# Optimization experiments

Hardware: AMD Instinct MI355X
Metric: run time of the kernel (lower is better)

## Reference

```python
import jax, jax.numpy as jnp
import numpy as np

N, E, D, H = 20000, 320000, 300, 2
NEG_SLOPE = 0.2  # PyG GATConv default LeakyReLU slope


def setup_inputs() -> dict:
    key = jax.random.key(0)
    ks = jax.random.split(key, 8)
    return {
        "x": jax.random.normal(ks[0], (N, D), dtype=jnp.float32),
        "edge_index": jax.random.randint(ks[1], (2, E), 0, N, dtype=jnp.int64),
        "W": jax.random.normal(ks[2], (D, H, D), dtype=jnp.float32) * 0.05,
        "att_src": jax.random.normal(ks[3], (H, D), dtype=jnp.float32) * 0.05,
        "att_dst": jax.random.normal(ks[4], (H, D), dtype=jnp.float32) * 0.05,
        "bias": jax.random.normal(ks[5], (D,), dtype=jnp.float32) * 0.05,
        "lin_w": jax.random.normal(ks[6], (D, 1), dtype=jnp.float32) * 0.05,
        "lin_b": jax.random.normal(ks[7], (1,), dtype=jnp.float32) * 0.05,
    }


def reference(x, edge_index, W, att_src, att_dst, bias, lin_w, lin_b):
    n = x.shape[0]
    # add self-loops (PyG GATConv default)
    loops = jnp.arange(n, dtype=edge_index.dtype)
    src = jnp.concatenate([edge_index[0], loops])  # [E+N]
    dst = jnp.concatenate([edge_index[1], loops])
    # per-head linear projection: [N, H, D]
    xp = jnp.einsum('nd,dhe->nhe', x, W)
    # per-node attention logits [N, H]
    a_src = jnp.sum(xp * att_src, axis=-1)
    a_dst = jnp.sum(xp * att_dst, axis=-1)
    # per-edge score, LeakyReLU, segment softmax over incoming edges of dst
    e = jax.nn.leaky_relu(a_src[src] + a_dst[dst], NEG_SLOPE)  # [Et, H]
    emax = jax.ops.segment_max(e, dst, num_segments=n)  # self-loops ensure non-empty
    ee = jnp.exp(e - emax[dst])
    denom = jax.ops.segment_sum(ee, dst, num_segments=n)
    alpha = ee / denom[dst]  # [Et, H]
    # weighted scatter-add aggregation
    msg = xp[src] * alpha[:, :, None]  # [Et, H, D]
    out = jax.ops.segment_sum(msg, dst, num_segments=n)  # [N, H, D]
    out = out.mean(axis=1) + bias  # concat=False -> head average, then bias
    out = jax.nn.relu(out)
    return out @ lin_w + lin_b  # [N, 1]
```

## Files before the change

### kernel.cpp

```cpp
#include <hip/hip_runtime.h>
#include <math.h>

#define Nn 20000
#define Ee 320000
#define Dd 300
#define Hh 2
#define Cc 600
#define KP 320
#define MP 20096
#define NP 640
#define SQ 640

typedef _Float16 f16;
typedef __attribute__((ext_vector_type(8))) _Float16 f16x8;
typedef __attribute__((ext_vector_type(4))) _Float16 f16x4;
typedef __attribute__((ext_vector_type(4))) float f32x4;

__device__ __forceinline__ float lrelu(float x) { return x > 0.f ? x : 0.2f * x; }

#define GLDS16(src, dst)                                                            \
  __builtin_amdgcn_global_load_lds(                                                 \
      (const __attribute__((address_space(1))) unsigned int*)(src),                 \
      (__attribute__((address_space(3))) unsigned int*)(dst), 16, 0, 0)

__global__ __launch_bounds__(256) void k_pre2(const float* __restrict__ W,
                                              const float* __restrict__ att_src,
                                              const float* __restrict__ att_dst,
                                              f16* __restrict__ Wh, float* __restrict__ vatt,
                                              int* __restrict__ cnt, float* __restrict__ dsum) {
  int idx = blockIdx.x * 256 + threadIdx.x;
  if (idx < Nn) {
    cnt[idx] = 0;
    *(float2*)(dsum + 2 * idx) = make_float2(0.f, 0.f);
  }
  {
    int c = idx % NP, k0 = (idx / NP) * 4;
    f16x4 h;
#pragma unroll
    for (int j = 0; j < 4; ++j) {
      int k = k0 + j;
      h[j] = (f16)((k < Dd && c < Cc) ? W[(size_t)k * Cc + c] : 0.f);
    }
    *(f16x4*)(Wh + (size_t)c * KP + k0) = h;
  }
  int wid = idx >> 6, ln = idx & 63;
  if (wid < Dd) {
    float s0 = 0.f, s1 = 0.f, t0 = 0.f, t1 = 0.f;
    for (int e = ln; e < Dd; e += 64) {
      float w0 = W[(size_t)wid * Cc + e];
      float w1 = W[(size_t)wid * Cc + Dd + e];
      s0 += w0 * att_src[e];  s1 += w1 * att_src[Dd + e];
      t0 += w0 * att_dst[e];  t1 += w1 * att_dst[Dd + e];
    }
    for (int o = 32; o > 0; o >>= 1) {
      s0 += __shfl_down(s0, o, 64); s1 += __shfl_down(s1, o, 64);
      t0 += __shfl_down(t0, o, 64); t1 += __shfl_down(t1, o, 64);
    }
    if (ln == 0) {
      vatt[wid * 4 + 0] = s0; vatt[wid * 4 + 1] = s1;
      vatt[wid * 4 + 2] = t0; vatt[wid * 4 + 3] = t1;
    }
  }
}

__global__ __launch_bounds__(256) void k_pre1(const float* __restrict__ x,
                                              const float* __restrict__ vatt,
                                              const int* __restrict__ ei,
                                              f16* __restrict__ xh,
                                              float* __restrict__ a_src, float* __restrict__ a_dst,
                                              int* __restrict__ cnt) {
  int gid = blockIdx.x * 256 + threadIdx.x;
  if (gid < Ee) atomicAdd(&cnt[ei[Ee + gid]], 1);
  int wv = threadIdx.x >> 6, ln = threadIdx.x & 63;
  int n = blockIdx.x * 4 + wv;
  if (n >= MP) return;
  if (n >= Nn) {
#pragma unroll
    for (int k = 0; k < 5; ++k) xh[(size_t)n * KP + ln + 64 * k] = (f16)0.f;
    return;
  }
  const float* xr = x + (size_t)n * Dd;
  float s0 = 0.f, s1 = 0.f, t0 = 0.f, t1 = 0.f;
#pragma unroll
  for (int k = 0; k < 5; ++k) {
    int d = ln + 64 * k;
    float xv = 0.f;
    if (d < Dd) {
      xv = xr[d];
      float4 vv = *(const float4*)(vatt + d * 4);
      s0 += xv * vv.x; s1 += xv * vv.y; t0 += xv * vv.z; t1 += xv * vv.w;
    }
    xh[(size_t)n * KP + d] = (f16)xv;
  }
  for (int o = 32; o > 0; o >>= 1) {
    s0 += __shfl_down(s0, o, 64); s1 += __shfl_down(s1, o, 64);
    t0 += __shfl_down(t0, o, 64); t1 += __shfl_down(t1, o, 64);
  }
  if (ln == 0) {
    a_src[n * 2 + 0] = s0; a_src[n * 2 + 1] = s1;
    a_dst[n * 2 + 0] = t0; a_dst[n * 2 + 1] = t1;
  }
}

__global__ __launch_bounds__(256) void k_mm(const f16* __restrict__ xh, const f16* __restrict__ Wh,
                                            f16* __restrict__ xq) {
  __shared__ __align__(16) f16 As[128 * 32];
  __shared__ __align__(16) f16 Bs[128 * 32];
  int m0 = blockIdx.x * 128, n0 = blockIdx.y * 128;
  int tid = threadIdx.x, wv = tid >> 6, lane = tid & 63;
  int wr = wv >> 1, wc = wv & 1;

  int r0a = 32 * wv + (lane >> 2);
  int ca  = ((lane & 3) ^ ((r0a >> 1) & 3)) * 8;
  int r0b = r0a + 16;
  int cb  = ((lane & 3) ^ ((r0b >> 1) & 3)) * 8;

  f32x4 acc[4][4] = {};
  for (int ks = 0; ks < KP / 32; ++ks) {
    __syncthreads();
    GLDS16(xh + (size_t)(m0 + r0a) * KP + ks * 32 + ca, As + (32 * wv) * 32);
    GLDS16(xh + (size_t)(m0 + r0b) * KP + ks * 32 + cb, As + (32 * wv + 16) * 32);
    GLDS16(Wh + (size_t)(n0 + r0a) * KP + ks * 32 + ca, Bs + (32 * wv) * 32);
    GLDS16(Wh + (size_t)(n0 + r0b) * KP + ks * 32 + cb, Bs + (32 * wv + 16) * 32);
    __syncthreads();

    f16x8 af[4], bf[4];
#pragma unroll
    for (int i = 0; i < 4; ++i) {
      int rA = wr * 64 + i * 16 + (lane & 15);
      int sA = (lane >> 4) ^ ((rA >> 1) & 3);
      af[i] = *(const f16x8*)&As[rA * 32 + sA * 8];
      int rB = wc * 64 + i * 16 + (lane & 15);
      int sB = (lane >> 4) ^ ((rB >> 1) & 3);
      bf[i] = *(const f16x8*)&Bs[rB * 32 + sB * 8];
    }
#pragma unroll
    for (int i = 0; i < 4; ++i)
#pragma unroll
      for (int j = 0; j < 4; ++j)
        acc[i][j] = __builtin_amdgcn_mfma_f32_16x16x32_f16(af[i], bf[j], acc[i][j], 0, 0, 0);
  }

#pragma unroll
  for (int i = 0; i < 4; ++i) {
#pragma unroll
    for (int j = 0; j < 4; ++j) {
      int col = n0 + wc * 64 + j * 16 + (lane & 15);
      if (col < Cc) {
        int rbase = m0 + wr * 64 + i * 16 + ((lane >> 4) * 4);
#pragma unroll
        for (int r = 0; r < 4; ++r) {
          int row = rbase + r;
          if (row < Nn) xq[(size_t)row * SQ + col] = (f16)acc[i][j][r];
        }
      }
    }
  }
}

__global__ __launch_bounds__(1024) void k_scan(const int* __restrict__ cnt,
                                               int* __restrict__ offs, int* __restrict__ cur) {
  __shared__ int wsum[16];
  int t = threadIdx.x, wv = t >> 6, ln = t & 63;
  int i0 = t * 20;
  int v[20];
  int tot = 0;
  if (i0 < Nn) {
    const int4* p = (const int4*)(cnt + i0);
#pragma unroll
    for (int q = 0; q < 5; ++q) {
      int4 w = p[q];
      v[4 * q] = w.x; v[4 * q + 1] = w.y; v[4 * q + 2] = w.z; v[4 * q + 3] = w.w;
    }
#pragma unroll
    for (int j = 0; j < 20; ++j) tot += v[j];
  }
  int s = tot;
  for (int o = 1; o < 64; o <<= 1) {
    int u = __shfl_up(s, o, 64);
    if (ln >= o) s += u;
  }
  if (ln == 63) wsum[wv] = s;
  __syncthreads();
  if (wv == 0) {
    int w = (ln < 16) ? wsum[ln] : 0;
    for (int o = 1; o < 16; o <<= 1) {
      int u = __shfl_up(w, o, 64);
      if (ln >= o) w += u;
    }
    if (ln < 16) wsum[ln] = w;
  }
  __syncthreads();
  if (i0 < Nn) {
    int run = (wv > 0 ? wsum[wv - 1] : 0) + (s - tot);
#pragma unroll
    for (int j = 0; j < 20; ++j) {
      offs[i0 + j] = run;
      cur[i0 + j] = run;
      run += v[j];
    }
  }
  if (t == 0) offs[Nn] = wsum[15];
}

__global__ void k_scatter(const int* __restrict__ ei,
                          const float* __restrict__ a_src, const float* __restrict__ a_dst,
                          int* __restrict__ cur, float* __restrict__ dsum,
                          float4* __restrict__ erec) {
  int e = blockIdx.x * 256 + threadIdx.x;
  if (e < Ee) {
    int s = ei[e], d = ei[Ee + e];
    float2 av = *(const float2*)(a_src + 2 * s);
    float2 bv = *(const float2*)(a_dst + 2 * d);
    float e0 = __expf(lrelu(av.x + bv.x));
    float e1 = __expf(lrelu(av.y + bv.y));
    int pos = atomicAdd(&cur[d], 1);
    erec[pos] = make_float4(__int_as_float(s), e0, e1, 0.f);
    atomicAdd(&dsum[2 * d + 0], e0);
    atomicAdd(&dsum[2 * d + 1], e1);
  }
}

__global__ __launch_bounds__(256) void k_agg(const f16* __restrict__ xq,
    const float4* __restrict__ erec,
    const float* __restrict__ a_src, const float* __restrict__ a_dst,
    const float* __restrict__ dsum, const int* __restrict__ offs,
    const float* __restrict__ bias, const float* __restrict__ lin_w,
    const float* __restrict__ lin_b, float* __restrict__ out) {
  __shared__ float sAgg[4][600];
  int tid = threadIdx.x, wv = tid >> 6, ln = tid & 63;
  int n = blockIdx.x * 4 + wv;
  int beg = offs[n], deg = offs[n + 1] - beg;
  float2 adv = *(const float2*)(a_dst + 2 * n);
  float2 asv = *(const float2*)(a_src + 2 * n);
  float sw0 = __expf(lrelu(asv.x + adv.x));
  float sw1 = __expf(lrelu(asv.y + adv.y));
  float2 dv = *(const float2*)(dsum + 2 * n);
  float inv0 = 1.f / (dv.x + sw0), inv1 = 1.f / (dv.y + sw1);

  float acc[12] = {};
  auto addrow = [&](const f16* row, float p0, float p1) {
#pragma unroll
    for (int k = 0; k < 3; ++k) {
      int c = 4 * ln + 256 * k;
      if (c < Cc) {
        f16x4 hv = *(const f16x4*)(row + c);
        float p = (c < Dd) ? p0 : p1;
        acc[4 * k + 0] += p * (float)hv[0];
        acc[4 * k + 1] += p * (float)hv[1];
        acc[4 * k + 2] += p * (float)hv[2];
        acc[4 * k + 3] += p * (float)hv[3];
      }
    }
  };

  int j = 0;
  for (; j + 4 <= deg; j += 4) {
    float4 r0 = erec[beg + j + 0];
    float4 r1 = erec[beg + j + 1];
    float4 r2 = erec[beg + j + 2];
    float4 r3 = erec[beg + j + 3];
    addrow(xq + (size_t)__float_as_int(r0.x) * SQ, r0.y * inv0, r0.z * inv1);
    addrow(xq + (size_t)__float_as_int(r1.x) * SQ, r1.y * inv0, r1.z * inv1);
    addrow(xq + (size_t)__float_as_int(r2.x) * SQ, r2.y * inv0, r2.z * inv1);
    addrow(xq + (size_t)__float_as_int(r3.x) * SQ, r3.y * inv0, r3.z * inv1);
  }
  for (; j < deg; ++j) {
    float4 r = erec[beg + j];
    addrow(xq + (size_t)__float_as_int(r.x) * SQ, r.y * inv0, r.z * inv1);
  }
  addrow(xq + (size_t)n * SQ, sw0 * inv0, sw1 * inv1);

#pragma unroll
  for (int k = 0; k < 3; ++k) {
    int c = 4 * ln + 256 * k;
    if (c < Cc) {
#pragma unroll
      for (int q = 0; q < 4; ++q) sAgg[wv][c + q] = acc[4 * k + q];
    }
  }
  __syncthreads();

  float part = 0.f;
#pragma unroll
  for (int k = 0; k < 5; ++k) {
    int d = ln + 64 * k;
    if (d < Dd) {
      float v = 0.5f * (sAgg[wv][d] + sAgg[wv][d + Dd]) + bias[d];
      v = fmaxf(v, 0.f);
      part += v * lin_w[d];
    }
  }
  for (int o = 32; o > 0; o >>= 1) part += __shfl_xor(part, o, 64);
  if (ln == 0) out[n] = part + lin_b[0];
}

extern "C" void kernel_launch(void* const* d_in, const int* in_sizes, int n_in,
                              void* d_out, int out_size, void* d_ws, size_t ws_size,
                              hipStream_t stream) {
  const float* x       = (const float*)d_in[0];
  const int*   ei      = (const int*)d_in[1];
  const float* W       = (const float*)d_in[2];
  const float* att_src = (const float*)d_in[3];
  const float* att_dst = (const float*)d_in[4];
  const float* bias    = (const float*)d_in[5];
  const float* lin_w   = (const float*)d_in[6];
  const float* lin_b   = (const float*)d_in[7];
  float* out = (float*)d_out;

  char* ws = (char*)d_ws;
  size_t off = 0;
  auto alloc = [&](size_t bytes) {
    void* p = ws + off;
    off = (off + bytes + 255) & ~(size_t)255;
    return p;
  };
  f16*    xq    = (f16*)alloc((size_t)Nn * SQ * 2);
  f16*    xh    = (f16*)alloc((size_t)MP * KP * 2);
  f16*    Wh    = (f16*)alloc((size_t)NP * KP * 2);
  float*  vatt  = (float*)alloc((size_t)Dd * 4 * 4);
  float*  a_src = (float*)alloc((size_t)Nn * Hh * 4);
  float*  a_dst = (float*)alloc((size_t)Nn * Hh * 4);
  int*    cnt   = (int*)alloc((size_t)Nn * 4);
  int*    offs  = (int*)alloc((size_t)(Nn + 1) * 4);
  int*    cur   = (int*)alloc((size_t)Nn * 4);
  float*  dsum  = (float*)alloc((size_t)Nn * 2 * 4);
  float4* erec  = (float4*)alloc((size_t)Ee * 16);

  k_pre2<<<NP * (KP / 4) / 256, 256, 0, stream>>>(W, att_src, att_dst, Wh, vatt, cnt, dsum);
  k_pre1<<<MP / 4, 256, 0, stream>>>(x, vatt, ei, xh, a_src, a_dst, cnt);
  k_mm<<<dim3(MP / 128, NP / 128), 256, 0, stream>>>(xh, Wh, xq);
  k_scan<<<1, 1024, 0, stream>>>(cnt, offs, cur);
  k_scatter<<<(Ee + 255) / 256, 256, 0, stream>>>(ei, a_src, a_dst, cur, dsum, erec);
  k_agg<<<Nn / 4, 256, 0, stream>>>(xq, erec, a_src, a_dst, dsum, offs, bias, lin_w, lin_b, out);
}
```

Before: 246.8 us.

## Replace denominator atomics with per-node reduction and degree-sort aggregation nodes

Drops the per-edge atomic accumulation of softmax denominators; each wave in the aggregation kernel now sums its node's edge weights with a wave reduction. The scan kernel also builds a degree-bucketed permutation of nodes so aggregation blocks process nodes of similar degree. The aim is to cut atomic contention and reduce load imbalance between waves in a block. In exchange, aggregation reads the edge records an extra time and the single-block scan does more shared-memory atomic work.

Result: faster. 222.4 us (-9.9%).

```diff
diff --git a/kernel.cpp b/kernel.cpp
--- a/kernel.cpp
+++ b/kernel.cpp
@@ -27,12 +27,9 @@
                                               const float* __restrict__ att_src,
                                               const float* __restrict__ att_dst,
                                               f16* __restrict__ Wh, float* __restrict__ vatt,
-                                              int* __restrict__ cnt, float* __restrict__ dsum) {
+                                              int* __restrict__ cnt) {
   int idx = blockIdx.x * 256 + threadIdx.x;
-  if (idx < Nn) {
-    cnt[idx] = 0;
-    *(float2*)(dsum + 2 * idx) = make_float2(0.f, 0.f);
-  }
+  if (idx < Nn) cnt[idx] = 0;
   {
     int c = idx % NP, k0 = (idx / NP) * 4;
     f16x4 h;
@@ -159,8 +156,11 @@
 }
 
 __global__ __launch_bounds__(1024) void k_scan(const int* __restrict__ cnt,
-                                               int* __restrict__ offs, int* __restrict__ cur) {
+                                               int* __restrict__ offs, int* __restrict__ cur,
+                                               int* __restrict__ perm) {
   __shared__ int wsum[16];
+  __shared__ int dhist[64];
+  __shared__ int dcur[64];
   int t = threadIdx.x, wv = t >> 6, ln = t & 63;
   int i0 = t * 20;
   int v[20];
@@ -175,6 +175,7 @@
 #pragma unroll
     for (int j = 0; j < 20; ++j) tot += v[j];
   }
+  if (t < 64) dhist[t] = 0;
   int s = tot;
   for (int o = 1; o < 64; o <<= 1) {
     int u = __shfl_up(s, o, 64);
@@ -182,6 +183,10 @@
   }
   if (ln == 63) wsum[wv] = s;
   __syncthreads();
+  if (i0 < Nn) {
+#pragma unroll
+    for (int j = 0; j < 20; ++j) atomicAdd(&dhist[min(v[j], 63)], 1);
+  }
   if (wv == 0) {
     int w = (ln < 16) ? wsum[ln] : 0;
     for (int o = 1; o < 16; o <<= 1) {
@@ -191,6 +196,16 @@
     if (ln < 16) wsum[ln] = w;
   }
   __syncthreads();
+  if (wv == 0) {
+    int h = dhist[ln];
+    int sc = h;
+    for (int o = 1; o < 64; o <<= 1) {
+      int u = __shfl_up(sc, o, 64);
+      if (ln >= o) sc += u;
+    }
+    dcur[ln] = sc - h;
+  }
+  __syncthreads();
   if (i0 < Nn) {
     int run = (wv > 0 ? wsum[wv - 1] : 0) + (s - tot);
 #pragma unroll
@@ -198,6 +213,8 @@
       offs[i0 + j] = run;
       cur[i0 + j] = run;
       run += v[j];
+      int pos = atomicAdd(&dcur[min(v[j], 63)], 1);
+      perm[pos] = i0 + j;
     }
   }
   if (t == 0) offs[Nn] = wsum[15];
@@ -205,8 +222,7 @@
 
 __global__ void k_scatter(const int* __restrict__ ei,
                           const float* __restrict__ a_src, const float* __restrict__ a_dst,
-                          int* __restrict__ cur, float* __restrict__ dsum,
-                          float4* __restrict__ erec) {
+                          int* __restrict__ cur, float4* __restrict__ erec) {
   int e = blockIdx.x * 256 + threadIdx.x;
   if (e < Ee) {
     int s = ei[e], d = ei[Ee + e];
@@ -216,27 +232,34 @@
     float e1 = __expf(lrelu(av.y + bv.y));
     int pos = atomicAdd(&cur[d], 1);
     erec[pos] = make_float4(__int_as_float(s), e0, e1, 0.f);
-    atomicAdd(&dsum[2 * d + 0], e0);
-    atomicAdd(&dsum[2 * d + 1], e1);
   }
 }
 
 __global__ __launch_bounds__(256) void k_agg(const f16* __restrict__ xq,
-    const float4* __restrict__ erec,
+    const float4* __restrict__ erec, const int* __restrict__ perm,
     const float* __restrict__ a_src, const float* __restrict__ a_dst,
-    const float* __restrict__ dsum, const int* __restrict__ offs,
+    const int* __restrict__ offs,
     const float* __restrict__ bias, const float* __restrict__ lin_w,
     const float* __restrict__ lin_b, float* __restrict__ out) {
   __shared__ float sAgg[4][600];
   int tid = threadIdx.x, wv = tid >> 6, ln = tid & 63;
-  int n = blockIdx.x * 4 + wv;
+  int n = perm[blockIdx.x * 4 + wv];
   int beg = offs[n], deg = offs[n + 1] - beg;
   float2 adv = *(const float2*)(a_dst + 2 * n);
   float2 asv = *(const float2*)(a_src + 2 * n);
   float sw0 = __expf(lrelu(asv.x + adv.x));
   float sw1 = __expf(lrelu(asv.y + adv.y));
-  float2 dv = *(const float2*)(dsum + 2 * n);
-  float inv0 = 1.f / (dv.x + sw0), inv1 = 1.f / (dv.y + sw1);
+
+  float t0 = 0.f, t1 = 0.f;
+  for (int i = ln; i < deg; i += 64) {
+    float4 r = erec[beg + i];
+    t0 += r.y; t1 += r.z;
+  }
+  for (int o = 32; o > 0; o >>= 1) {
+    t0 += __shfl_xor(t0, o, 64);
+    t1 += __shfl_xor(t1, o, 64);
+  }
+  float inv0 = 1.f / (t0 + sw0), inv1 = 1.f / (t1 + sw1);
 
   float acc[12] = {};
   auto addrow = [&](const f16* row, float p0, float p1) {
@@ -324,13 +347,13 @@
   int*    cnt   = (int*)alloc((size_t)Nn * 4);
   int*    offs  = (int*)alloc((size_t)(Nn + 1) * 4);
   int*    cur   = (int*)alloc((size_t)Nn * 4);
-  float*  dsum  = (float*)alloc((size_t)Nn * 2 * 4);
+  int*    perm  = (int*)alloc((size_t)Nn * 4);
   float4* erec  = (float4*)alloc((size_t)Ee * 16);
 
-  k_pre2<<<NP * (KP / 4) / 256, 256, 0, stream>>>(W, att_src, att_dst, Wh, vatt, cnt, dsum);
+  k_pre2<<<NP * (KP / 4) / 256, 256, 0, stream>>>(W, att_src, att_dst, Wh, vatt, cnt);
   k_pre1<<<MP / 4, 256, 0, stream>>>(x, vatt, ei, xh, a_src, a_dst, cnt);
   k_mm<<<dim3(MP / 128, NP / 128), 256, 0, stream>>>(xh, Wh, xq);
-  k_scan<<<1, 1024, 0, stream>>>(cnt, offs, cur);
-  k_scatter<<<(Ee + 255) / 256, 256, 0, stream>>>(ei, a_src, a_dst, cur, dsum, erec);
-  k_agg<<<Nn / 4, 256, 0, stream>>>(xq, erec, a_src, a_dst, dsum, offs, bias, lin_w, lin_b, out);
-}
+  k_scan<<<1, 1024, 0, stream>>>(cnt, offs, cur, perm);
+  k_scatter<<<(Ee + 255) / 256, 256, 0, stream>>>(ei, a_src, a_dst, cur, erec);
+  k_agg<<<Nn / 4, 256, 0, stream>>>(xq, erec, perm, a_src, a_dst, offs, bias, lin_w, lin_b, out);
+}
```

## Merge GEMM and edge scatter into one launch, compute softmax denominators in aggregation

Applied to the files above, without the earlier changes.

The GEMM kernel and the edge-scatter kernel are fused into a single launch, with block ranges split by role so the scatter work can run alongside the matrix multiply. The per-destination atomic accumulation of the softmax denominators is removed. Each aggregation wave now sums the unnormalised edge weights itself and scales the result once at the end. Edge records shrink from 16-byte float4 to 8 bytes by storing the two exp weights as fp16. This cuts atomic traffic and memory bandwidth, at the cost of some precision in the attention weights and possible fp16 overflow for large logits.

After: 208.8 us. -15.4%, faster.

```diff
diff --git a/kernel.cpp b/kernel.cpp
--- a/kernel.cpp
+++ b/kernel.cpp
@@ -1,5 +1,6 @@
 #include <hip/hip_runtime.h>
 #include <math.h>
+#include <string.h>
 
 #define Nn 20000
 #define Ee 320000
@@ -10,6 +11,7 @@
 #define MP 20096
 #define NP 640
 #define SQ 640
+#define MMB 785
 
 typedef _Float16 f16;
 typedef __attribute__((ext_vector_type(8))) _Float16 f16x8;
@@ -27,12 +29,9 @@
                                               const float* __restrict__ att_src,
                                               const float* __restrict__ att_dst,
                                               f16* __restrict__ Wh, float* __restrict__ vatt,
-                                              int* __restrict__ cnt, float* __restrict__ dsum) {
+                                              int* __restrict__ cnt) {
   int idx = blockIdx.x * 256 + threadIdx.x;
-  if (idx < Nn) {
-    cnt[idx] = 0;
-    *(float2*)(dsum + 2 * idx) = make_float2(0.f, 0.f);
-  }
+  if (idx < Nn) cnt[idx] = 0;
   {
     int c = idx % NP, k0 = (idx / NP) * 4;
     f16x4 h;
@@ -102,62 +101,6 @@
   }
 }
 
-__global__ __launch_bounds__(256) void k_mm(const f16* __restrict__ xh, const f16* __restrict__ Wh,
-                                            f16* __restrict__ xq) {
-  __shared__ __align__(16) f16 As[128 * 32];
-  __shared__ __align__(16) f16 Bs[128 * 32];
-  int m0 = blockIdx.x * 128, n0 = blockIdx.y * 128;
-  int tid = threadIdx.x, wv = tid >> 6, lane = tid & 63;
-  int wr = wv >> 1, wc = wv & 1;
-
-  int r0a = 32 * wv + (lane >> 2);
-  int ca  = ((lane & 3) ^ ((r0a >> 1) & 3)) * 8;
-  int r0b = r0a + 16;
-  int cb  = ((lane & 3) ^ ((r0b >> 1) & 3)) * 8;
-
-  f32x4 acc[4][4] = {};
-  for (int ks = 0; ks < KP / 32; ++ks) {
-    __syncthreads();
-    GLDS16(xh + (size_t)(m0 + r0a) * KP + ks * 32 + ca, As + (32 * wv) * 32);
-    GLDS16(xh + (size_t)(m0 + r0b) * KP + ks * 32 + cb, As + (32 * wv + 16) * 32);
-    GLDS16(Wh + (size_t)(n0 + r0a) * KP + ks * 32 + ca, Bs + (32 * wv) * 32);
-    GLDS16(Wh + (size_t)(n0 + r0b) * KP + ks * 32 + cb, Bs + (32 * wv + 16) * 32);
-    __syncthreads();
-
-    f16x8 af[4], bf[4];
-#pragma unroll
-    for (int i = 0; i < 4; ++i) {
-      int rA = wr * 64 + i * 16 + (lane & 15);
-      int sA = (lane >> 4) ^ ((rA >> 1) & 3);
-      af[i] = *(const f16x8*)&As[rA * 32 + sA * 8];
-      int rB = wc * 64 + i * 16 + (lane & 15);
-      int sB = (lane >> 4) ^ ((rB >> 1) & 3);
-      bf[i] = *(const f16x8*)&Bs[rB * 32 + sB * 8];
-    }
-#pragma unroll
-    for (int i = 0; i < 4; ++i)
-#pragma unroll
-      for (int j = 0; j < 4; ++j)
-        acc[i][j] = __builtin_amdgcn_mfma_f32_16x16x32_f16(af[i], bf[j], acc[i][j], 0, 0, 0);
-  }
-
-#pragma unroll
-  for (int i = 0; i < 4; ++i) {
-#pragma unroll
-    for (int j = 0; j < 4; ++j) {
-      int col = n0 + wc * 64 + j * 16 + (lane & 15);
-      if (col < Cc) {
-        int rbase = m0 + wr * 64 + i * 16 + ((lane >> 4) * 4);
-#pragma unroll
-        for (int r = 0; r < 4; ++r) {
-          int row = rbase + r;
-          if (row < Nn) xq[(size_t)row * SQ + col] = (f16)acc[i][j][r];
-        }
-      }
-    }
-  }
-}
-
 __global__ __launch_bounds__(1024) void k_scan(const int* __restrict__ cnt,
                                                int* __restrict__ offs, int* __restrict__ cur) {
   __shared__ int wsum[16];
@@ -203,28 +146,89 @@
   if (t == 0) offs[Nn] = wsum[15];
 }
 
-__global__ void k_scatter(const int* __restrict__ ei,
-                          const float* __restrict__ a_src, const float* __restrict__ a_dst,
-                          int* __restrict__ cur, float* __restrict__ dsum,
-                          float4* __restrict__ erec) {
-  int e = blockIdx.x * 256 + threadIdx.x;
-  if (e < Ee) {
-    int s = ei[e], d = ei[Ee + e];
-    float2 av = *(const float2*)(a_src + 2 * s);
-    float2 bv = *(const float2*)(a_dst + 2 * d);
-    float e0 = __expf(lrelu(av.x + bv.x));
-    float e1 = __expf(lrelu(av.y + bv.y));
-    int pos = atomicAdd(&cur[d], 1);
-    erec[pos] = make_float4(__int_as_float(s), e0, e1, 0.f);
-    atomicAdd(&dsum[2 * d + 0], e0);
-    atomicAdd(&dsum[2 * d + 1], e1);
+__global__ __launch_bounds__(256) void k_mid(const f16* __restrict__ xh, const f16* __restrict__ Wh,
+                                             f16* __restrict__ xq,
+                                             const int* __restrict__ ei,
+                                             const float* __restrict__ a_src,
+                                             const float* __restrict__ a_dst,
+                                             int* __restrict__ cur, uint2* __restrict__ erec) {
+  __shared__ __align__(16) f16 As[128 * 32];
+  __shared__ __align__(16) f16 Bs[128 * 32];
+  int bid = blockIdx.x, tid = threadIdx.x;
+
+  if (bid >= MMB) {
+    int e = (bid - MMB) * 256 + tid;
+    if (e < Ee) {
+      int s = ei[e], d = ei[Ee + e];
+      float2 av = *(const float2*)(a_src + 2 * s);
+      float2 bv = *(const float2*)(a_dst + 2 * d);
+      f16 h0 = (f16)__expf(lrelu(av.x + bv.x));
+      f16 h1 = (f16)__expf(lrelu(av.y + bv.y));
+      unsigned short u0, u1;
+      __builtin_memcpy(&u0, &h0, 2);
+      __builtin_memcpy(&u1, &h1, 2);
+      int pos = atomicAdd(&cur[d], 1);
+      erec[pos] = make_uint2((unsigned)s, ((unsigned)u1 << 16) | u0);
+    }
+    return;
+  }
+
+  int m0 = (bid % 157) * 128, n0 = (bid / 157) * 128;
+  int wv = tid >> 6, lane = tid & 63;
+  int wr = wv >> 1, wc = wv & 1;
+
+  int r0a = 32 * wv + (lane >> 2);
+  int ca  = ((lane & 3) ^ ((r0a >> 1) & 3)) * 8;
+  int r0b = r0a + 16;
+  int cb  = ((lane & 3) ^ ((r0b >> 1) & 3)) * 8;
+
+  f32x4 acc[4][4] = {};
+  for (int ks = 0; ks < KP / 32; ++ks) {
+    __syncthreads();
+    GLDS16(xh + (size_t)(m0 + r0a) * KP + ks * 32 + ca, As + (32 * wv) * 32);
+    GLDS16(xh + (size_t)(m0 + r0b) * KP + ks * 32 + cb, As + (32 * wv + 16) * 32);
+    GLDS16(Wh + (size_t)(n0 + r0a) * KP + ks * 32 + ca, Bs + (32 * wv) * 32);
+    GLDS16(Wh + (size_t)(n0 + r0b) * KP + ks * 32 + cb, Bs + (32 * wv + 16) * 32);
+    __syncthreads();
+
+    f16x8 af[4], bf[4];
+#pragma unroll
+    for (int i = 0; i < 4; ++i) {
+      int rA = wr * 64 + i * 16 + (lane & 15);
+      int sA = (lane >> 4) ^ ((rA >> 1) & 3);
+      af[i] = *(const f16x8*)&As[rA * 32 + sA * 8];
+      int rB = wc * 64 + i * 16 + (lane & 15);
+      int sB = (lane >> 4) ^ ((rB >> 1) & 3);
+      bf[i] = *(const f16x8*)&Bs[rB * 32 + sB * 8];
+    }
+#pragma unroll
+    for (int i = 0; i < 4; ++i)
+#pragma unroll
+      for (int j = 0; j < 4; ++j)
+        acc[i][j] = __builtin_amdgcn_mfma_f32_16x16x32_f16(af[i], bf[j], acc[i][j], 0, 0, 0);
+  }
+
+#pragma unroll
+  for (int i = 0; i < 4; ++i) {
+#pragma unroll
+    for (int j = 0; j < 4; ++j) {
+      int col = n0 + wc * 64 + j * 16 + (lane & 15);
+      if (col < Cc) {
+        int rbase = m0 + wr * 64 + i * 16 + ((lane >> 4) * 4);
+#pragma unroll
+        for (int r = 0; r < 4; ++r) {
+          int row = rbase + r;
+          if (row < Nn) xq[(size_t)row * SQ + col] = (f16)acc[i][j][r];
+        }
+      }
+    }
   }
 }
 
 __global__ __launch_bounds__(256) void k_agg(const f16* __restrict__ xq,
-    const float4* __restrict__ erec,
+    const uint2* __restrict__ erec,
     const float* __restrict__ a_src, const float* __restrict__ a_dst,
-    const float* __restrict__ dsum, const int* __restrict__ offs,
+    const int* __restrict__ offs,
     const float* __restrict__ bias, const float* __restrict__ lin_w,
     const float* __restrict__ lin_b, float* __restrict__ out) {
   __shared__ float sAgg[4][600];
@@ -235,10 +239,16 @@
   float2 asv = *(const float2*)(a_src + 2 * n);
   float sw0 = __expf(lrelu(asv.x + adv.x));
   float sw1 = __expf(lrelu(asv.y + adv.y));
-  float2 dv = *(const float2*)(dsum + 2 * n);
-  float inv0 = 1.f / (dv.x + sw0), inv1 = 1.f / (dv.y + sw1);
 
   float acc[12] = {};
+  float t0 = 0.f, t1 = 0.f;
+  auto unpack = [](unsigned w, float& e0, float& e1) {
+    unsigned short q0 = (unsigned short)(w & 0xffff), q1 = (unsigned short)(w >> 16);
+    f16 h0, h1;
+    __builtin_memcpy(&h0, &q0, 2);
+    __builtin_memcpy(&h1, &q1, 2);
+    e0 = (float)h0; e1 = (float)h1;
+  };
   auto addrow = [&](const f16* row, float p0, float p1) {
 #pragma unroll
     for (int k = 0; k < 3; ++k) {
@@ -256,27 +266,37 @@
 
   int j = 0;
   for (; j + 4 <= deg; j += 4) {
-    float4 r0 = erec[beg + j + 0];
-    float4 r1 = erec[beg + j + 1];
-    float4 r2 = erec[beg + j + 2];
-    float4 r3 = erec[beg + j + 3];
-    addrow(xq + (size_t)__float_as_int(r0.x) * SQ, r0.y * inv0, r0.z * inv1);
-    addrow(xq + (size_t)__float_as_int(r1.x) * SQ, r1.y * inv0, r1.z * inv1);
-    addrow(xq + (size_t)__float_as_int(r2.x) * SQ, r2.y * inv0, r2.z * inv1);
-    addrow(xq + (size_t)__float_as_int(r3.x) * SQ, r3.y * inv0, r3.z * inv1);
+    uint2 r0 = erec[beg + j + 0];
+    uint2 r1 = erec[beg + j + 1];
+    uint2 r2 = erec[beg + j + 2];
+    uint2 r3 = erec[beg + j + 3];
+    float e00, e01, e10, e11, e20, e21, e30, e31;
+    unpack(r0.y, e00, e01); unpack(r1.y, e10, e11);
+    unpack(r2.y, e20, e21); unpack(r3.y, e30, e31);
+    t0 += e00 + e10 + e20 + e30;
+    t1 += e01 + e11 + e21 + e31;
+    addrow(xq + (size_t)r0.x * SQ, e00, e01);
+    addrow(xq + (size_t)r1.x * SQ, e10, e11);
+    addrow(xq + (size_t)r2.x * SQ, e20, e21);
+    addrow(xq + (size_t)r3.x * SQ, e30, e31);
   }
   for (; j < deg; ++j) {
-    float4 r = erec[beg + j];
-    addrow(xq + (size_t)__float_as_int(r.x) * SQ, r.y * inv0, r.z * inv1);
-  }
-  addrow(xq + (size_t)n * SQ, sw0 * inv0, sw1 * inv1);
-
+    uint2 r = erec[beg + j];
+    float e0, e1;
+    unpack(r.y, e0, e1);
+    t0 += e0; t1 += e1;
+    addrow(xq + (size_t)r.x * SQ, e0, e1);
+  }
+  addrow(xq + (size_t)n * SQ, sw0, sw1);
+
+  float inv0 = 1.f / (t0 + sw0), inv1 = 1.f / (t1 + sw1);
 #pragma unroll
   for (int k = 0; k < 3; ++k) {
     int c = 4 * ln + 256 * k;
     if (c < Cc) {
-#pragma unroll
-      for (int q = 0; q < 4; ++q) sAgg[wv][c + q] = acc[4 * k + q];
+      float p = (c < Dd) ? inv0 : inv1;
+#pragma unroll
+      for (int q = 0; q < 4; ++q) sAgg[wv][c + q] = acc[4 * k + q] * p;
     }
   }
   __syncthreads();
@@ -315,22 +335,20 @@
     off = (off + bytes + 255) & ~(size_t)255;
     return p;
   };
-  f16*    xq    = (f16*)alloc((size_t)Nn * SQ * 2);
-  f16*    xh    = (f16*)alloc((size_t)MP * KP * 2);
-  f16*    Wh    = (f16*)alloc((size_t)NP * KP * 2);
-  float*  vatt  = (float*)alloc((size_t)Dd * 4 * 4);
-  float*  a_src = (float*)alloc((size_t)Nn * Hh * 4);
-  float*  a_dst = (float*)alloc((size_t)Nn * Hh * 4);
-  int*    cnt   = (int*)alloc((size_t)Nn * 4);
-  int*    offs  = (int*)alloc((size_t)(Nn + 1) * 4);
-  int*    cur   = (int*)alloc((size_t)Nn * 4);
-  float*  dsum  = (float*)alloc((size_t)Nn * 2 * 4);
-  float4* erec  = (float4*)alloc((size_t)Ee * 16);
-
-  k_pre2<<<NP * (KP / 4) / 256, 256, 0, stream>>>(W, att_src, att_dst, Wh, vatt, cnt, dsum);
+  f16*   xq    = (f16*)alloc((size_t)Nn * SQ * 2);
+  f16*   xh    = (f16*)alloc((size_t)MP * KP * 2);
+  f16*   Wh    = (f16*)alloc((size_t)NP * KP * 2);
+  float* vatt  = (float*)alloc((size_t)Dd * 4 * 4);
+  float* a_src = (float*)alloc((size_t)Nn * Hh * 4);
+  float* a_dst = (float*)alloc((size_t)Nn * Hh * 4);
+  int*   cnt   = (int*)alloc((size_t)Nn * 4);
+  int*   offs  = (int*)alloc((size_t)(Nn + 1) * 4);
+  int*   cur   = (int*)alloc((size_t)Nn * 4);
+  uint2* erec  = (uint2*)alloc((size_t)Ee * 8);
+
+  k_pre2<<<NP * (KP / 4) / 256, 256, 0, stream>>>(W, att_src, att_dst, Wh, vatt, cnt);
   k_pre1<<<MP / 4, 256, 0, stream>>>(x, vatt, ei, xh, a_src, a_dst, cnt);
-  k_mm<<<dim3(MP / 128, NP / 128), 256, 0, stream>>>(xh, Wh, xq);
   k_scan<<<1, 1024, 0, stream>>>(cnt, offs, cur);
-  k_scatter<<<(Ee + 255) / 256, 256, 0, stream>>>(ei, a_src, a_dst, cur, dsum, erec);
-  k_agg<<<Nn / 4, 256, 0, stream>>>(xq, erec, a_src, a_dst, dsum, offs, bias, lin_w, lin_b, out);
-}
+  k_mid<<<MMB + (Ee + 255) / 256, 256, 0, stream>>>(xh, Wh, xq, ei, a_src, a_dst, cur, erec);
+  k_agg<<<Nn / 4, 256, 0, stream>>>(xq, erec, a_src, a_dst, offs, bias, lin_w, lin_b, out);
+}
```
